# Kernel tuning notes

Measured on AMD Instinct MI355X. Metric: run time of the kernel, lower is better.

Reference implementation:

```python
import jax, jax.numpy as jnp
import numpy as np

B, N, C_IN = 4, 48, 32
HID = [32, 32]          # hidden_channel_list
NB = [32, 32]           # neighborhood_channels
C_OUT = 16
N_BASIS = 6             # equivariant 2->2 basis ops used by SnConv2


def _masked(t, mask):
    # zero out entries for padded nodes; mask: B,n,n,n bool, t: B,n,n,n,C
    return jnp.where(mask[..., None], t, jnp.zeros((), t.dtype))


def snconv2(t, W, b):
    """Sn-equivariant 2nd-order conv on dims (1,2); dim 3 rides along.
    t: B,i,j,m,C.  W: [6, C_in, C_out], one mixing matrix per basis op."""
    n = t.shape[1]
    tT = jnp.swapaxes(t, 1, 2)                       # transpose op
    diag = jnp.einsum('biimc->bimc', t)              # diagonal, B,i,m,C
    rows = t.sum(axis=2) / n                         # row sums,  B,i,m,C
    cols = t.sum(axis=1) / n                         # col sums,  B,j,m,C
    tot = t.sum(axis=(1, 2)) / (n * n)               # total sum, B,m,C
    # contract small features BEFORE broadcasting back to 2nd order
    out = (jnp.einsum('bijmc,cd->bijmd', t, W[0])
           + jnp.einsum('bijmc,cd->bijmd', tT, W[1])
           + jnp.einsum('bimc,cd->bimd', diag, W[2])[:, :, None]
           + jnp.einsum('bimc,cd->bimd', rows, W[3])[:, :, None]
           + jnp.einsum('bjmc,cd->bjmd', cols, W[4])[:, None]
           + jnp.einsum('bmc,cd->bmd', tot, W[5])[:, None, None]
           + b)
    return out


def localconv2(t, Wv, bv, Ww, bw, Wo, bo):
    """LocalConv2, product_type='elementwise': per-channel message passing
    along the node dims: z[b,i,j] = sum_k v[b,i,k] * w[b,k,j] / n."""
    n = t.shape[1]
    v = jnp.einsum('bijmc,cd->bijmd', t, Wv) + bv
    w = jnp.einsum('bijmc,cd->bijmd', t, Ww) + bw
    z = jnp.einsum('bikmc,bkjmc->bijmc', v, w) / n
    return jnp.einsum('bijmc,cd->bijmd', z, Wo) + bo


def setup_inputs() -> dict:
    key = jax.random.key(0)
    ks = jax.random.split(key, 24)
    x = jax.random.normal(ks[0], (B, N, C_IN), dtype=jnp.float32)
    # graphs of unequal size: per-graph node counts in [N//2, N]
    sizes = jax.random.randint(ks[1], (B,), N // 2, N + 1)
    node_valid = jnp.arange(N)[None, :] < sizes[:, None]            # B,n
    mask = (node_valid[:, :, None, None]
            & node_valid[:, None, :, None]
            & node_valid[:, None, None, :])                          # B,n,n,n
    s = 0.05
    inp = {'x': x, 'mask': mask}
    cin = C_IN
    for li, (nch, cout) in enumerate(zip(NB, HID)):
        inp[f'basic_W{li}'] = s * jax.random.normal(ks[2 + 8 * li], (N_BASIS, cin, cin), dtype=jnp.float32)
        inp[f'basic_b{li}'] = jnp.zeros((cin,), jnp.float32)
        inp[f'lv_W{li}'] = s * jax.random.normal(ks[3 + 8 * li], (cin, nch), dtype=jnp.float32)
        inp[f'lv_b{li}'] = jnp.zeros((nch,), jnp.float32)
        inp[f'lw_W{li}'] = s * jax.random.normal(ks[4 + 8 * li], (cin, nch), dtype=jnp.float32)
        inp[f'lw_b{li}'] = jnp.zeros((nch,), jnp.float32)
        inp[f'lo_W{li}'] = s * jax.random.normal(ks[5 + 8 * li], (nch, cout), dtype=jnp.float32)
        inp[f'lo_b{li}'] = jnp.zeros((cout,), jnp.float32)
        cin = cout
    inp['final_W'] = s * jax.random.normal(ks[20], (N_BASIS, cin, C_OUT), dtype=jnp.float32)
    inp['final_b'] = jnp.zeros((C_OUT,), jnp.float32)
    return inp


def reference(x, mask,
              basic_W0, basic_b0, lv_W0, lv_b0, lw_W0, lw_b0, lo_W0, lo_b0,
              basic_W1, basic_b1, lv_W1, lv_b1, lw_W1, lw_b1, lo_W1, lo_b1,
              final_W, final_b):
    # order-3 outer product T[b,i,j,k,c] = x[b,i,c]*x[b,j,c]*x[b,k,c]
    t = (x[:, :, None, None, :] * x[:, None, :, None, :]) * x[:, None, None, :, :]
    t = _masked(t, mask)
    layers = [(basic_W0, basic_b0, lv_W0, lv_b0, lw_W0, lw_b0, lo_W0, lo_b0),
              (basic_W1, basic_b1, lv_W1, lv_b1, lw_W1, lw_b1, lo_W1, lo_b1)]
    for bw_, bb_, vw, vb, ww, wb, ow, ob in layers:
        t = _masked(snconv2(t, bw_, bb_), mask)
        t = localconv2(t, vw, vb, ww, wb, ow, ob)
        t = jax.nn.relu(t)
        t = _masked(t, mask)
    out = _masked(snconv2(t, final_W, final_b), mask)
    return out
```

## Files before the change

### kernel.cpp

```cpp
#include <hip/hip_runtime.h>
#include <cstdint>


namespace {

constexpr int nB = 4, nN = 48, nC = 32;
constexpr int SJ_ = nN * nC;
constexpr int SI_ = nN * SJ_;
constexpr long SB_ = (long)nN * SI_;
constexpr int RP_ = 294912;
constexpr int CP_ = 294912;
constexpr int TP_ = 6144;

__device__ __forceinline__ void decodePos(int p, int& b, int& i, int& j, int& m) {
    m = p % nN; int r = p / nN;
    j = r % nN; r /= nN;
    i = r % nN; b = r / nN;
}

__global__ __launch_bounds__(256) void k_prep(const float* __restrict__ x,
                                              const void* __restrict__ maskp,
                                              float* __restrict__ vm,
                                              float* __restrict__ S)
{
    __shared__ float vmL[nB * nN];
    const int tid = threadIdx.x;
    const unsigned int w0 = *(const unsigned int*)maskp;
    const bool is_byte = (w0 == 0x01010101u);
    if (tid < nB * nN) {
        int b = tid / nN, i = tid % nN;
        long idx = ((long)(b * nN + i) * nN + i) * nN + i;
        int bit;
        if (is_byte) bit = (((const unsigned char*)maskp)[idx] != 0);
        else         bit = (((const int*)maskp)[idx] != 0);
        float f = bit ? 1.f : 0.f;
        vm[tid] = f; vmL[tid] = f;
    }
    __syncthreads();
    if (tid < nB * nC) {
        int b = tid >> 5, c = tid & 31;
        float s = 0.f;
        for (int j = 0; j < nN; ++j) s += x[(b * nN + j) * nC + c] * vmL[b * nN + j];
        S[tid] = s;
    }
}

__global__ __launch_bounds__(256) void k_compose(
    const float* __restrict__ Wb0, const float* __restrict__ bb0,
    const float* __restrict__ Wv0, const float* __restrict__ Ww0,
    const float* __restrict__ Wb1, const float* __restrict__ bb1,
    const float* __restrict__ Wv1, const float* __restrict__ Ww1,
    float* __restrict__ cW, float* __restrict__ cb, float* __restrict__ cWs)
{
    const int blk = blockIdx.x;
    const float* Wb = (blk < 2) ? Wb0 : Wb1;
    const float* bb = (blk < 2) ? bb0 : bb1;
    const float* Wr = (blk == 0) ? Wv0 : (blk == 1) ? Ww0 : (blk == 2) ? Wv1 : Ww1;
    __shared__ float Ws[1024];
    const int tid = threadIdx.x;
    for (int q = tid; q < 1024; q += 256) Ws[q] = Wr[q];
    __syncthreads();
    for (int q = tid; q < 6144; q += 256) {
        const int d = q & 31;
        const float* row = Wb + (q >> 5) * 32;
        float s = 0.f;
        #pragma unroll
        for (int e = 0; e < 32; ++e) s = fmaf(row[e], Ws[e * 32 + d], s);
        cW[blk * 6144 + q] = s;
    }
    if (blk < 2) {
        for (int q = tid; q < 1024; q += 256) {
            const int d = q & 31; const int c = q >> 5;
            const float* r0 = Wb + c * 32;
            const float* r1 = Wb + 1024 + c * 32;
            float s = 0.f;
            #pragma unroll
            for (int e = 0; e < 32; ++e) s = fmaf(r0[e] + r1[e], Ws[e * 32 + d], s);
            cWs[blk * 1024 + q] = s;
        }
    }
    if (tid < 32) {
        float s = 0.f;
        #pragma unroll
        for (int e = 0; e < 32; ++e) s = fmaf(bb[e], Ws[e * 32 + tid], s);
        cb[blk * 32 + tid] = s;
    }
}

__global__ __launch_bounds__(256) void k_mix0(
    const float* __restrict__ x, const float* __restrict__ S,
    const float* __restrict__ Wb, const float* __restrict__ bias,
    float* __restrict__ drp, float* __restrict__ ccp, float* __restrict__ tbp)
{
    __shared__ float W2s[1024], W3s[1024], W4s[1024], W5s[1024], bs[32];
    const int tid = threadIdx.x;
    for (int q = tid; q < 1024; q += 256) {
        W2s[q] = Wb[2048 + q]; W3s[q] = Wb[3072 + q];
        W4s[q] = Wb[4096 + q]; W5s[q] = Wb[5120 + q];
    }
    if (tid < 32) bs[tid] = bias[tid];
    __syncthreads();
    const int id = blockIdx.x * 256 + tid;
    const int m = id % nN; int r = id / nN; const int i = r % nN; const int b = r / nN;
    float odr[32], occ[32];
    #pragma unroll
    for (int d = 0; d < 32; ++d) { odr[d] = 0.f; occ[d] = 0.f; }
    for (int c2 = 0; c2 < 32; ++c2) {
        float xi = x[(b * nN + i) * nC + c2];
        float xm = x[(b * nN + m) * nC + c2];
        float sc = S[b * nC + c2];
        float A = xi * xi * xm;
        float R = xi * xm * sc * (1.f / nN);
        #pragma unroll
        for (int d = 0; d < 32; ++d) {
            odr[d] = fmaf(A, W2s[c2 * 32 + d], fmaf(R, W3s[c2 * 32 + d], odr[d]));
            occ[d] = fmaf(R, W4s[c2 * 32 + d], occ[d]);
        }
    }
    #pragma unroll
    for (int d = 0; d < 32; d += 4) {
        *(float4*)(drp + (size_t)id * 32 + d) = make_float4(odr[d], odr[d+1], odr[d+2], odr[d+3]);
        *(float4*)(ccp + (size_t)id * 32 + d) = make_float4(occ[d], occ[d+1], occ[d+2], occ[d+3]);
    }
    if (i == 0) {
        float ot[32];
        #pragma unroll
        for (int d = 0; d < 32; ++d) ot[d] = bs[d];
        for (int c2 = 0; c2 < 32; ++c2) {
            float xm = x[(b * nN + m) * nC + c2];
            float sc = S[b * nC + c2];
            float Tc = xm * sc * sc * (1.f / (nN * nN));
            #pragma unroll
            for (int d = 0; d < 32; ++d) ot[d] = fmaf(Tc, W5s[c2 * 32 + d], ot[d]);
        }
        for (int d = 0; d < 32; d += 4)
            *(float4*)(tbp + (size_t)(b * nN + m) * 32 + d) = make_float4(ot[d], ot[d+1], ot[d+2], ot[d+3]);
    }
}

template <int DOUT>
__global__ __launch_bounds__(256) void k_mix(
    const float* __restrict__ dgp, const float* __restrict__ rw2,
    const float* __restrict__ cl2, const float* __restrict__ tt4,
    const float* __restrict__ Wb, const float* __restrict__ bias,
    float* __restrict__ drp, float* __restrict__ ccp, float* __restrict__ tbp)
{
    __shared__ float W2s[32 * DOUT], W3s[32 * DOUT], W4s[32 * DOUT], W5s[32 * DOUT], bs[DOUT];
    const int tid = threadIdx.x;
    for (int q = tid; q < 32 * DOUT; q += 256) {
        W2s[q] = Wb[2 * 32 * DOUT + q]; W3s[q] = Wb[3 * 32 * DOUT + q];
        W4s[q] = Wb[4 * 32 * DOUT + q]; W5s[q] = Wb[5 * 32 * DOUT + q];
    }
    if (tid < DOUT) bs[tid] = bias[tid];
    __syncthreads();
    const int id = blockIdx.x * 256 + tid;
    const int m = id % nN; int r = id / nN; const int i = r % nN; const int b = r / nN;
    float odr[DOUT], occ[DOUT];
    #pragma unroll
    for (int d = 0; d < DOUT; ++d) { odr[d] = 0.f; occ[d] = 0.f; }
    for (int c2 = 0; c2 < 32; ++c2) {
        size_t q = (size_t)id * 32 + c2;
        float dg = dgp[q];
        float rw = (rw2[q] + rw2[q + RP_]) * (1.f / nN);
        float cl = (cl2[q] + cl2[q + CP_]) * (1.f / nN);
        #pragma unroll
        for (int d = 0; d < DOUT; ++d) {
            odr[d] = fmaf(dg, W2s[c2 * DOUT + d], fmaf(rw, W3s[c2 * DOUT + d], odr[d]));
            occ[d] = fmaf(cl, W4s[c2 * DOUT + d], occ[d]);
        }
    }
    #pragma unroll
    for (int d = 0; d < DOUT; d += 4) {
        *(float4*)(drp + (size_t)id * DOUT + d) = make_float4(odr[d], odr[d+1], odr[d+2], odr[d+3]);
        *(float4*)(ccp + (size_t)id * DOUT + d) = make_float4(occ[d], occ[d+1], occ[d+2], occ[d+3]);
    }
    if (i == 0) {
        float ot[DOUT];
        #pragma unroll
        for (int d = 0; d < DOUT; ++d) ot[d] = bs[d];
        for (int c2 = 0; c2 < 32; ++c2) {
            size_t q = (size_t)(b * nN + m) * 32 + c2;
            float tv = (tt4[q] + tt4[q + TP_] + tt4[q + 2 * TP_] + tt4[q + 3 * TP_])
                       * (1.f / (nN * nN));
            #pragma unroll
            for (int d = 0; d < DOUT; ++d) ot[d] = fmaf(tv, W5s[c2 * DOUT + d], ot[d]);
        }
        for (int d = 0; d < DOUT; d += 4)
            *(float4*)(tbp + (size_t)(b * nN + m) * DOUT + d) = make_float4(ot[d], ot[d+1], ot[d+2], ot[d+3]);
    }
}

#define FMA4(ar, tv, w4)                       \
    ar[0] = fmaf(tv, w4.x, ar[0]);             \
    ar[1] = fmaf(tv, w4.y, ar[1]);             \
    ar[2] = fmaf(tv, w4.z, ar[2]);             \
    ar[3] = fmaf(tv, w4.w, ar[3]);

template <int MODE>
__global__ __launch_bounds__(256) void k_vw(
    const float* __restrict__ src, const float* __restrict__ vm,
    const float* __restrict__ drv, const float* __restrict__ ccv, const float* __restrict__ tbv,
    const float* __restrict__ drw, const float* __restrict__ ccw, const float* __restrict__ tbw,
    const float* __restrict__ Wv2, const float* __restrict__ Ww2,
    const float* __restrict__ bv, const float* __restrict__ bw,
    float* __restrict__ vout, float* __restrict__ wout)
{
    __shared__ float sA[128 * 34];
    __shared__ float sB[(MODE == 0) ? 4 : 128 * 34];
    __shared__ float wL[(MODE == 0) ? 2048 : 4096];
    const int tid = threadIdx.x;
    const long base = (long)blockIdx.x * 128;

    {
        float4* wl4 = (float4*)wL;
        if (MODE == 0) {
            for (int q = tid; q < 512; q += 256) wl4[q] = ((const float4*)Wv2)[q];
        } else {
            for (int q = tid; q < 512; q += 256) wl4[q] = ((const float4*)Wv2)[q];
            for (int q = tid; q < 512; q += 256) wl4[512 + q] = ((const float4*)Ww2)[q];
        }
    }
    if (MODE == 0) {
        for (int rep = 0; rep < 4; ++rep) {
            int q = rep * 256 + tid; int pl = q >> 3, cq = q & 7;
            int p = (int)base + pl;
            int b, i, j, m; decodePos(p, b, i, j, m);
            float4 xi = *(const float4*)(src + (size_t)(b * nN + i) * nC + cq * 4);
            float4 xj = *(const float4*)(src + (size_t)(b * nN + j) * nC + cq * 4);
            float4 xm = *(const float4*)(src + (size_t)(b * nN + m) * nC + cq * 4);
            int o = pl * 34 + cq * 4;
            sA[o + 0] = xi.x * xj.x * xm.x;
            sA[o + 1] = xi.y * xj.y * xm.y;
            sA[o + 2] = xi.z * xj.z * xm.z;
            sA[o + 3] = xi.w * xj.w * xm.w;
        }
    } else {
        for (int rep = 0; rep < 4; ++rep) {
            int q = rep * 256 + tid; int pl = q >> 3, cq = q & 7;
            long p = base + pl;
            float4 a = *(const float4*)(src + p * nC + cq * 4);
            int o = pl * 34 + cq * 4;
            sA[o + 0] = a.x; sA[o + 1] = a.y; sA[o + 2] = a.z; sA[o + 3] = a.w;
            int b, i, j, m; decodePos((int)p, b, i, j, m);
            long pT = ((long)(b * nN + j) * nN + i) * nN + m;
            float4 t4 = *(const float4*)(src + pT * nC + cq * 4);
            sB[o + 0] = t4.x; sB[o + 1] = t4.y; sB[o + 2] = t4.z; sB[o + 3] = t4.w;
        }
    }
    __syncthreads();

    const int pt = tid >> 3, dq = tid & 7;
    const int p0 = pt * 4, d0 = dq * 4;
    float accv[4][4], accw[4][4];
    #pragma unroll
    for (int l = 0; l < 4; ++l)
        #pragma unroll
        for (int d = 0; d < 4; ++d) { accv[l][d] = 0.f; accw[l][d] = 0.f; }

    auto sweep_dual = [&](const float* sp, const float* wv_, const float* ww_) {
        #pragma unroll
        for (int cp = 0; cp < 16; ++cp) {
            float2 t0 = *(const float2*)(sp + (p0 + 0) * 34 + cp * 2);
            float2 t1 = *(const float2*)(sp + (p0 + 1) * 34 + cp * 2);
            float2 t2 = *(const float2*)(sp + (p0 + 2) * 34 + cp * 2);
            float2 t3 = *(const float2*)(sp + (p0 + 3) * 34 + cp * 2);
            const int c0 = cp * 2, c1 = cp * 2 + 1;
            float4 wv0 = *(const float4*)(wv_ + c0 * nC + d0);
            float4 wv1 = *(const float4*)(wv_ + c1 * nC + d0);
            float4 ww0 = *(const float4*)(ww_ + c0 * nC + d0);
            float4 ww1 = *(const float4*)(ww_ + c1 * nC + d0);
            FMA4(accv[0], t0.x, wv0); FMA4(accv[1], t1.x, wv0);
            FMA4(accv[2], t2.x, wv0); FMA4(accv[3], t3.x, wv0);
            FMA4(accv[0], t0.y, wv1); FMA4(accv[1], t1.y, wv1);
            FMA4(accv[2], t2.y, wv1); FMA4(accv[3], t3.y, wv1);
            FMA4(accw[0], t0.x, ww0); FMA4(accw[1], t1.x, ww0);
            FMA4(accw[2], t2.x, ww0); FMA4(accw[3], t3.x, ww0);
            FMA4(accw[0], t0.y, ww1); FMA4(accw[1], t1.y, ww1);
            FMA4(accw[2], t2.y, ww1); FMA4(accw[3], t3.y, ww1);
        }
    };

    if (MODE == 0) {
        sweep_dual(sA, wL, wL + 1024);
    } else {
        sweep_dual(sA, wL, wL + 2048);
        sweep_dual(sB, wL + 1024, wL + 3072);
    }

    __builtin_amdgcn_sched_barrier(0);
    {
        float4 b4 = *(const float4*)(bv + d0);
        #pragma unroll
        for (int l = 0; l < 4; ++l) {
            int p = (int)base + p0 + l;
            int b, i, j, m; decodePos(p, b, i, j, m);
            float4 d4 = *(const float4*)(drv + (size_t)((b * nN + i) * nN + m) * nC + d0);
            float4 c4 = *(const float4*)(ccv + (size_t)((b * nN + j) * nN + m) * nC + d0);
            float4 t4 = *(const float4*)(tbv + (size_t)(b * nN + m) * nC + d0);
            float mk = vm[b * nN + i] * vm[b * nN + j] * vm[b * nN + m];
            float4 o4;
            o4.x = (accv[l][0] + d4.x + c4.x + t4.x) * mk + b4.x;
            o4.y = (accv[l][1] + d4.y + c4.y + t4.y) * mk + b4.y;
            o4.z = (accv[l][2] + d4.z + c4.z + t4.z) * mk + b4.z;
            o4.w = (accv[l][3] + d4.w + c4.w + t4.w) * mk + b4.w;
            *(float4*)(vout + (size_t)(base + p0 + l) * nC + d0) = o4;
        }
    }
    __builtin_amdgcn_sched_barrier(0);
    {
        float4 b4 = *(const float4*)(bw + d0);
        #pragma unroll
        for (int l = 0; l < 4; ++l) {
            int p = (int)base + p0 + l;
            int b, i, j, m; decodePos(p, b, i, j, m);
            float4 d4 = *(const float4*)(drw + (size_t)((b * nN + i) * nN + m) * nC + d0);
            float4 c4 = *(const float4*)(ccw + (size_t)((b * nN + j) * nN + m) * nC + d0);
            float4 t4 = *(const float4*)(tbw + (size_t)(b * nN + m) * nC + d0);
            float mk = vm[b * nN + i] * vm[b * nN + j] * vm[b * nN + m];
            float4 o4;
            o4.x = (accw[l][0] + d4.x + c4.x + t4.x) * mk + b4.x;
            o4.y = (accw[l][1] + d4.y + c4.y + t4.y) * mk + b4.y;
            o4.z = (accw[l][2] + d4.z + c4.z + t4.z) * mk + b4.z;
            o4.w = (accw[l][3] + d4.w + c4.w + t4.w) * mk + b4.w;
            *(float4*)(wout + (size_t)(base + p0 + l) * nC + d0) = o4;
        }
    }
}

__global__ __launch_bounds__(256, 3) void k_z(
    const float* __restrict__ v, const float* __restrict__ w,
    const float* __restrict__ Wo, const float* __restrict__ bo,
    const float* __restrict__ vm, float* __restrict__ tout,
    float* __restrict__ rows2, float* __restrict__ cols2,
    float* __restrict__ diag_, float* __restrict__ tot4)
{
    __shared__ float lds[12912];
    float* Vt = lds;
    float* Wt = lds + 6456;
    constexpr int ZS = 34;
    constexpr int ZWO = 9792;
    constexpr int TOT0 = 10816;
    const int tid = threadIdx.x;
    const int blk = blockIdx.x;
    const int tl = blk & 3; const int bm = blk >> 2;
    const int it = tl >> 1, jt = tl & 1;
    const int b = bm / nN, m = bm % nN;
    const int c = tid & 31;
    const int g = tid >> 5;
    const int i3 = g >> 1, j2 = g & 1;
    const int il0 = i3 * 6, jl0 = j2 * 12;
    const size_t posbase = (size_t)b * SB_ + (size_t)m * nC;

    float acc[6][12];
    #pragma unroll
    for (int l = 0; l < 6; ++l)
        #pragma unroll
        for (int u = 0; u < 12; ++u) acc[l][u] = 0.f;

    for (int kc = 0; kc < 6; ++kc) {
        if (kc) __syncthreads();
        #pragma unroll
        for (int rr = 0; rr < 6; ++rr) {
            int q = rr * 256 + tid; int pos = q >> 3, cq = q & 7;
            int ii = pos >> 3, kk = pos & 7;
            float4 a = *(const float4*)(v + posbase + (size_t)(it * 24 + ii) * SI_
                                          + (size_t)(kc * 8 + kk) * SJ_ + cq * 4);
            float* dst = Vt + kk * 807 + (cq * 4) * 25 + ii;
            dst[0] = a.x; dst[25] = a.y; dst[50] = a.z; dst[75] = a.w;
        }
        #pragma unroll
        for (int rr = 0; rr < 6; ++rr) {
            int q = rr * 256 + tid; int pos = q >> 3, cq = q & 7;
            int kk = pos / 24, jj = pos - kk * 24;
            float4 a = *(const float4*)(w + posbase + (size_t)(kc * 8 + kk) * SI_
                                          + (size_t)(jt * 24 + jj) * SJ_ + cq * 4);
            float* dst = Wt + kk * 807 + (cq * 4) * 25 + jj;
            dst[0] = a.x; dst[25] = a.y; dst[50] = a.z; dst[75] = a.w;
        }
        __syncthreads();
        #pragma unroll
        for (int kk = 0; kk < 8; ++kk) {
            float vf[6], wf[12];
            #pragma unroll
            for (int l = 0; l < 6; ++l) vf[l] = Vt[kk * 807 + c * 25 + il0 + l];
            #pragma unroll
            for (int u = 0; u < 12; ++u) wf[u] = Wt[kk * 807 + c * 25 + jl0 + u];
            #pragma unroll
            for (int l = 0; l < 6; ++l)
                #pragma unroll
                for (int u = 0; u < 12; ++u)
                    acc[l][u] = fmaf(vf[l], wf[u], acc[l][u]);
        }
    }
    __syncthreads();

    #pragma unroll
    for (int e = 0; e < 4; ++e)
        lds[ZWO + e * 256 + tid] = Wo[e * 256 + tid] * (1.f / nN);

    const int ptE = tid >> 3, dqE = tid & 7, d0 = dqE * 4;
    const float4 b4 = *(const float4*)(bo + d0);
    const float vmm = vm[b * nN + m];
    float colacc[3] = {0.f, 0.f, 0.f};
    float totacc = 0.f;

    for (int h = 0; h < 2; ++h) {
        if (h) __syncthreads();
        if ((i3 >> 1) == h) {
            int r0 = il0 - 12 * h;
            #pragma unroll
            for (int l = 0; l < 6; ++l)
                #pragma unroll
                for (int u = 0; u < 12; ++u)
                    lds[((r0 + l) * 24 + jl0 + u) * ZS + c] = acc[l][u];
        }
        __syncthreads();

        float oac[9][4];
        #pragma unroll
        for (int u = 0; u < 9; ++u)
            #pragma unroll
            for (int d = 0; d < 4; ++d) oac[u][d] = 0.f;
        #pragma unroll
        for (int c2 = 0; c2 < 32; ++c2) {
            float4 wo4 = *(const float4*)(lds + ZWO + c2 * 32 + d0);
            float zv[9];
            #pragma unroll
            for (int u = 0; u < 9; ++u) zv[u] = lds[(ptE * 9 + u) * ZS + c2];
            #pragma unroll
            for (int u = 0; u < 9; ++u) {
                oac[u][0] = fmaf(zv[u], wo4.x, oac[u][0]);
                oac[u][1] = fmaf(zv[u], wo4.y, oac[u][1]);
                oac[u][2] = fmaf(zv[u], wo4.z, oac[u][2]);
                oac[u][3] = fmaf(zv[u], wo4.w, oac[u][3]);
            }
        }
        __syncthreads();

        #pragma unroll
        for (int u = 0; u < 9; ++u) {
            int p = ptE * 9 + u;
            int rl = p / 24, jl = p - rl * 24;
            int gi = it * 24 + 12 * h + rl, gj = jt * 24 + jl;
            float mk = vm[b * nN + gi] * vm[b * nN + gj] * vmm;
            float4 o4;
            o4.x = fmaxf(oac[u][0] + b4.x, 0.f) * mk;
            o4.y = fmaxf(oac[u][1] + b4.y, 0.f) * mk;
            o4.z = fmaxf(oac[u][2] + b4.z, 0.f) * mk;
            o4.w = fmaxf(oac[u][3] + b4.w, 0.f) * mk;
            *(float4*)(tout + posbase + (size_t)gi * SI_ + (size_t)gj * SJ_ + d0) = o4;
            *(float2*)(lds + p * ZS + d0) = make_float2(o4.x, o4.y);
            *(float2*)(lds + p * ZS + d0 + 2) = make_float2(o4.z, o4.w);
        }
        __syncthreads();

        for (int rd = 0; rd < 2; ++rd) {
            int task = rd * 256 + tid;
            if (task < 384) {
                int i_r = task >> 5, c_r = task & 31;
                float rsum = 0.f;
                #pragma unroll
                for (int jl = 0; jl < 24; ++jl) rsum += lds[(i_r * 24 + jl) * ZS + c_r];
                int gi = it * 24 + 12 * h + i_r;
                rows2[(size_t)jt * RP_ + ((size_t)(b * nN + gi) * nN + m) * nC + c_r] = rsum;
                totacc += rsum;
                if (it == jt)
                    diag_[((size_t)(b * nN + gi) * nN + m) * nC + c_r] =
                        lds[(i_r * 24 + (12 * h + i_r)) * ZS + c_r];
            }
        }
        #pragma unroll
        for (int rr = 0; rr < 3; ++rr) {
            int task = rr * 256 + tid;
            int jl = task >> 5, c_c = task & 31;
            float csum = 0.f;
            #pragma unroll
            for (int il = 0; il < 12; ++il) csum += lds[(il * 24 + jl) * ZS + c_c];
            colacc[rr] += csum;
        }
    }

    #pragma unroll
    for (int rr = 0; rr < 3; ++rr) {
        int task = rr * 256 + tid;
        int jl = task >> 5, c_c = task & 31;
        cols2[(size_t)it * CP_ + ((size_t)(b * nN + jt * 24 + jl) * nN + m) * nC + c_c] = colacc[rr];
    }
    lds[TOT0 + g * 32 + c] = totacc;
    __syncthreads();
    if (tid < 32) {
        float s = 0.f;
        #pragma unroll
        for (int gg = 0; gg < 8; ++gg) s += lds[TOT0 + gg * 32 + tid];
        tot4[(size_t)(it * 2 + jt) * TP_ + (size_t)(b * nN + m) * nC + tid] = s;
    }
}

__global__ __launch_bounds__(256) void k_final(
    const float* __restrict__ t, const float* __restrict__ vm,
    const float* __restrict__ drp, const float* __restrict__ ccp, const float* __restrict__ tbp,
    const float* __restrict__ W0, const float* __restrict__ W1,
    float* __restrict__ out)
{
    __shared__ float sA[128 * 34], sB[128 * 34];
    const int tid = threadIdx.x;
    const long base = (long)blockIdx.x * 128;
    for (int rep = 0; rep < 4; ++rep) {
        int q = rep * 256 + tid; int pl = q >> 3, cq = q & 7;
        long p = base + pl;
        float4 a = *(const float4*)(t + p * nC + cq * 4);
        int o = pl * 34 + cq * 4;
        sA[o + 0] = a.x; sA[o + 1] = a.y; sA[o + 2] = a.z; sA[o + 3] = a.w;
        int b, i, j, m; decodePos((int)p, b, i, j, m);
        long pT = ((long)(b * nN + j) * nN + i) * nN + m;
        float4 t4 = *(const float4*)(t + pT * nC + cq * 4);
        sB[o + 0] = t4.x; sB[o + 1] = t4.y; sB[o + 2] = t4.z; sB[o + 3] = t4.w;
    }
    __syncthreads();
    const int pt = tid >> 3, dq = tid & 7;
    const int p0 = pt * 4, d0 = dq * 2;
    float wc[32][2], acc[4][2];
    #pragma unroll
    for (int l = 0; l < 4; ++l) { acc[l][0] = 0.f; acc[l][1] = 0.f; }

    auto loadW = [&](const float* Wp) {
        #pragma unroll
        for (int c2 = 0; c2 < 32; ++c2) {
            float2 q2 = *(const float2*)(Wp + c2 * 16 + d0);
            wc[c2][0] = q2.x; wc[c2][1] = q2.y;
        }
    };
    auto sweep = [&](const float* sp) {
        #pragma unroll
        for (int cp = 0; cp < 16; ++cp) {
            float2 t0 = *(const float2*)(sp + (p0 + 0) * 34 + cp * 2);
            float2 t1 = *(const float2*)(sp + (p0 + 1) * 34 + cp * 2);
            float2 t2 = *(const float2*)(sp + (p0 + 2) * 34 + cp * 2);
            float2 t3 = *(const float2*)(sp + (p0 + 3) * 34 + cp * 2);
            const int c0 = cp * 2, c1 = cp * 2 + 1;
            acc[0][0] = fmaf(t0.x, wc[c0][0], acc[0][0]); acc[0][1] = fmaf(t0.x, wc[c0][1], acc[0][1]);
            acc[1][0] = fmaf(t1.x, wc[c0][0], acc[1][0]); acc[1][1] = fmaf(t1.x, wc[c0][1], acc[1][1]);
            acc[2][0] = fmaf(t2.x, wc[c0][0], acc[2][0]); acc[2][1] = fmaf(t2.x, wc[c0][1], acc[2][1]);
            acc[3][0] = fmaf(t3.x, wc[c0][0], acc[3][0]); acc[3][1] = fmaf(t3.x, wc[c0][1], acc[3][1]);
            acc[0][0] = fmaf(t0.y, wc[c1][0], acc[0][0]); acc[0][1] = fmaf(t0.y, wc[c1][1], acc[0][1]);
            acc[1][0] = fmaf(t1.y, wc[c1][0], acc[1][0]); acc[1][1] = fmaf(t1.y, wc[c1][1], acc[1][1]);
            acc[2][0] = fmaf(t2.y, wc[c1][0], acc[2][0]); acc[2][1] = fmaf(t2.y, wc[c1][1], acc[2][1]);
            acc[3][0] = fmaf(t3.y, wc[c1][0], acc[3][0]); acc[3][1] = fmaf(t3.y, wc[c1][1], acc[3][1]);
        }
    };

    loadW(W0); sweep(sA);
    loadW(W1); sweep(sB);

    #pragma unroll
    for (int l = 0; l < 4; ++l) {
        int p = (int)base + p0 + l;
        int b, i, j, m; decodePos(p, b, i, j, m);
        float2 d2 = *(const float2*)(drp + (size_t)((b * nN + i) * nN + m) * 16 + d0);
        float2 cc2 = *(const float2*)(ccp + (size_t)((b * nN + j) * nN + m) * 16 + d0);
        float2 tb2 = *(const float2*)(tbp + (size_t)(b * nN + m) * 16 + d0);
        float mk = vm[b * nN + i] * vm[b * nN + j] * vm[b * nN + m];
        float2 o2;
        o2.x = (acc[l][0] + d2.x + cc2.x + tb2.x) * mk;
        o2.y = (acc[l][1] + d2.y + cc2.y + tb2.y) * mk;
        *(float2*)(out + (size_t)p * 16 + d0) = o2;
    }
}

}

extern "C" void kernel_launch(void* const* d_in, const int* in_sizes, int n_in,
                              void* d_out, int out_size, void* d_ws, size_t ws_size,
                              hipStream_t stream)
{
    (void)in_sizes; (void)n_in; (void)out_size; (void)ws_size;
    const float* x    = (const float*)d_in[0];
    const void*  mask = d_in[1];
    const float* bW0  = (const float*)d_in[2];
    const float* bb0  = (const float*)d_in[3];
    const float* lvW0 = (const float*)d_in[4];
    const float* lvb0 = (const float*)d_in[5];
    const float* lwW0 = (const float*)d_in[6];
    const float* lwb0 = (const float*)d_in[7];
    const float* loW0 = (const float*)d_in[8];
    const float* lob0 = (const float*)d_in[9];
    const float* bW1  = (const float*)d_in[10];
    const float* bb1  = (const float*)d_in[11];
    const float* lvW1 = (const float*)d_in[12];
    const float* lvb1 = (const float*)d_in[13];
    const float* lwW1 = (const float*)d_in[14];
    const float* lwb1 = (const float*)d_in[15];
    const float* loW1 = (const float*)d_in[16];
    const float* lob1 = (const float*)d_in[17];
    const float* fW   = (const float*)d_in[18];
    const float* fb   = (const float*)d_in[19];

    float* ws  = (float*)d_ws;
    float* t     = ws;
    float* v     = ws + 14155776L;
    float* w     = ws + 28311552L;
    float* rows2 = ws + 42467328L;
    float* cols2 = rows2 + 2 * 294912;
    float* diag  = cols2 + 2 * 294912;
    float* tot4  = diag + 294912;
    float* drv   = tot4 + 4 * 6144;
    float* ccv   = drv + 294912;
    float* tbv   = ccv + 294912;
    float* drw   = tbv + 6144;
    float* ccw   = drw + 294912;
    float* tbw   = ccw + 294912;
    float* cW    = tbw + 6144;
    float* cb    = cW + 4 * 6144;
    float* cWs   = cb + 128;
    float* S     = cWs + 2048;
    float* vm    = S + 128;
    float* out   = (float*)d_out;

    k_prep<<<1, 256, 0, stream>>>(x, mask, vm, S);
    k_compose<<<4, 256, 0, stream>>>(bW0, bb0, lvW0, lwW0, bW1, bb1, lvW1, lwW1, cW, cb, cWs);

    k_mix0<<<36, 256, 0, stream>>>(x, S, cW + 0,    cb + 0,  drv, ccv, tbv);
    k_mix0<<<36, 256, 0, stream>>>(x, S, cW + 6144, cb + 32, drw, ccw, tbw);
    k_vw<0><<<3456, 256, 0, stream>>>(x, vm, drv, ccv, tbv, drw, ccw, tbw,
                                      cWs,
                                      cWs,
                                      lvb0, lwb0, v, w);
    k_z<<<768, 256, 0, stream>>>(v, w, loW0, lob0, vm, t, rows2, cols2, diag, tot4);

    k_mix<32><<<36, 256, 0, stream>>>(diag, rows2, cols2, tot4, cW + 12288, cb + 64, drv, ccv, tbv);
    k_mix<32><<<36, 256, 0, stream>>>(diag, rows2, cols2, tot4, cW + 18432, cb + 96, drw, ccw, tbw);
    k_vw<1><<<3456, 256, 0, stream>>>(t, vm, drv, ccv, tbv, drw, ccw, tbw,
                                      cW + 12288,
                                      cW + 18432,
                                      lvb1, lwb1, v, w);
    k_z<<<768, 256, 0, stream>>>(v, w, loW1, lob1, vm, t, rows2, cols2, diag, tot4);

    k_mix<16><<<36, 256, 0, stream>>>(diag, rows2, cols2, tot4, fW, fb, drv, ccv, tbv);
    k_final<<<3456, 256, 0, stream>>>(t, vm, drv, ccv, tbv, fW, fW + 512, out);
}
```

Baseline: 547.8 us.

## Persistent double-buffered chunk loop in vw/final kernels and merge small launches

The k_vw and k_final kernels become persistent-style blocks. Each block processes 9 chunks of 64 positions with a register-staged double buffer in LDS, so the global loads for the next chunk overlap the FMA sweep on the current one. Grid size drops from 3456 to 768 blocks. Separately, prep and compose are merged into one launch, and the paired mix kernels are merged into single launches with a block-index switch, cutting launch count. The cost is fewer positions per thread per chunk (2 instead of 4), which lowers weight reuse from registers, plus extra register pressure from the staged loads.

```diff
diff --git a/kernel.cpp b/kernel.cpp
--- a/kernel.cpp
+++ b/kernel.cpp
@@ -18,46 +18,45 @@
     i = r % nN; b = r / nN;
 }
 
-__global__ __launch_bounds__(256) void k_prep(const float* __restrict__ x,
-                                              const void* __restrict__ maskp,
-                                              float* __restrict__ vm,
-                                              float* __restrict__ S)
-{
-    __shared__ float vmL[nB * nN];
-    const int tid = threadIdx.x;
-    const unsigned int w0 = *(const unsigned int*)maskp;
-    const bool is_byte = (w0 == 0x01010101u);
-    if (tid < nB * nN) {
-        int b = tid / nN, i = tid % nN;
-        long idx = ((long)(b * nN + i) * nN + i) * nN + i;
-        int bit;
-        if (is_byte) bit = (((const unsigned char*)maskp)[idx] != 0);
-        else         bit = (((const int*)maskp)[idx] != 0);
-        float f = bit ? 1.f : 0.f;
-        vm[tid] = f; vmL[tid] = f;
-    }
-    __syncthreads();
-    if (tid < nB * nC) {
-        int b = tid >> 5, c = tid & 31;
-        float s = 0.f;
-        for (int j = 0; j < nN; ++j) s += x[(b * nN + j) * nC + c] * vmL[b * nN + j];
-        S[tid] = s;
-    }
-}
-
-__global__ __launch_bounds__(256) void k_compose(
+__global__ __launch_bounds__(256) void k_prepcomp(
+    const float* __restrict__ x, const void* __restrict__ maskp,
+    float* __restrict__ vm, float* __restrict__ S,
     const float* __restrict__ Wb0, const float* __restrict__ bb0,
     const float* __restrict__ Wv0, const float* __restrict__ Ww0,
     const float* __restrict__ Wb1, const float* __restrict__ bb1,
     const float* __restrict__ Wv1, const float* __restrict__ Ww1,
     float* __restrict__ cW, float* __restrict__ cb, float* __restrict__ cWs)
 {
+    __shared__ float Ws[1024];
+    __shared__ float vmL[nB * nN];
+    const int tid = threadIdx.x;
+
+    if (blockIdx.x == 4) {
+        const unsigned int w0 = *(const unsigned int*)maskp;
+        const bool is_byte = (w0 == 0x01010101u);
+        if (tid < nB * nN) {
+            int b = tid / nN, i = tid % nN;
+            long idx = ((long)(b * nN + i) * nN + i) * nN + i;
+            int bit;
+            if (is_byte) bit = (((const unsigned char*)maskp)[idx] != 0);
+            else         bit = (((const int*)maskp)[idx] != 0);
+            float f = bit ? 1.f : 0.f;
+            vm[tid] = f; vmL[tid] = f;
+        }
+        __syncthreads();
+        if (tid < nB * nC) {
+            int b = tid >> 5, c = tid & 31;
+            float s = 0.f;
+            for (int j = 0; j < nN; ++j) s += x[(b * nN + j) * nC + c] * vmL[b * nN + j];
+            S[tid] = s;
+        }
+        return;
+    }
+
     const int blk = blockIdx.x;
     const float* Wb = (blk < 2) ? Wb0 : Wb1;
     const float* bb = (blk < 2) ? bb0 : bb1;
     const float* Wr = (blk == 0) ? Wv0 : (blk == 1) ? Ww0 : (blk == 2) ? Wv1 : Ww1;
-    __shared__ float Ws[1024];
-    const int tid = threadIdx.x;
     for (int q = tid; q < 1024; q += 256) Ws[q] = Wr[q];
     __syncthreads();
     for (int q = tid; q < 6144; q += 256) {
@@ -89,9 +88,17 @@
 
 __global__ __launch_bounds__(256) void k_mix0(
     const float* __restrict__ x, const float* __restrict__ S,
-    const float* __restrict__ Wb, const float* __restrict__ bias,
-    float* __restrict__ drp, float* __restrict__ ccp, float* __restrict__ tbp)
+    const float* __restrict__ Wb_a, const float* __restrict__ bias_a,
+    float* __restrict__ dr_a, float* __restrict__ cc_a, float* __restrict__ tb_a,
+    const float* __restrict__ Wb_b, const float* __restrict__ bias_b,
+    float* __restrict__ dr_b, float* __restrict__ cc_b, float* __restrict__ tb_b)
 {
+    const int set = (blockIdx.x >= 36);
+    const float* Wb   = set ? Wb_b   : Wb_a;
+    const float* bias = set ? bias_b : bias_a;
+    float* drp = set ? dr_b : dr_a;
+    float* ccp = set ? cc_b : cc_a;
+    float* tbp = set ? tb_b : tb_a;
     __shared__ float W2s[1024], W3s[1024], W4s[1024], W5s[1024], bs[32];
     const int tid = threadIdx.x;
     for (int q = tid; q < 1024; q += 256) {
@@ -100,7 +107,7 @@
     }
     if (tid < 32) bs[tid] = bias[tid];
     __syncthreads();
-    const int id = blockIdx.x * 256 + tid;
+    const int id = (blockIdx.x - (set ? 36 : 0)) * 256 + tid;
     const int m = id % nN; int r = id / nN; const int i = r % nN; const int b = r / nN;
     float odr[32], occ[32];
     #pragma unroll
@@ -142,9 +149,17 @@
 __global__ __launch_bounds__(256) void k_mix(
     const float* __restrict__ dgp, const float* __restrict__ rw2,
     const float* __restrict__ cl2, const float* __restrict__ tt4,
-    const float* __restrict__ Wb, const float* __restrict__ bias,
-    float* __restrict__ drp, float* __restrict__ ccp, float* __restrict__ tbp)
+    const float* __restrict__ Wb_a, const float* __restrict__ bias_a,
+    float* __restrict__ dr_a, float* __restrict__ cc_a, float* __restrict__ tb_a,
+    const float* __restrict__ Wb_b, const float* __restrict__ bias_b,
+    float* __restrict__ dr_b, float* __restrict__ cc_b, float* __restrict__ tb_b)
 {
+    const int set = (blockIdx.x >= 36);
+    const float* Wb   = set ? Wb_b   : Wb_a;
+    const float* bias = set ? bias_b : bias_a;
+    float* drp = set ? dr_b : dr_a;
+    float* ccp = set ? cc_b : cc_a;
+    float* tbp = set ? tb_b : tb_a;
     __shared__ float W2s[32 * DOUT], W3s[32 * DOUT], W4s[32 * DOUT], W5s[32 * DOUT], bs[DOUT];
     const int tid = threadIdx.x;
     for (int q = tid; q < 32 * DOUT; q += 256) {
@@ -153,7 +168,7 @@
     }
     if (tid < DOUT) bs[tid] = bias[tid];
     __syncthreads();
-    const int id = blockIdx.x * 256 + tid;
+    const int id = (blockIdx.x - (set ? 36 : 0)) * 256 + tid;
     const int m = id % nN; int r = id / nN; const int i = r % nN; const int b = r / nN;
     float odr[DOUT], occ[DOUT];
     #pragma unroll
@@ -205,124 +220,169 @@
     const float* __restrict__ bv, const float* __restrict__ bw,
     float* __restrict__ vout, float* __restrict__ wout)
 {
-    __shared__ float sA[128 * 34];
-    __shared__ float sB[(MODE == 0) ? 4 : 128 * 34];
+    constexpr int CH = 64;
+    constexpr int CS = CH * 34;
+    constexpr int BUF = (MODE == 0) ? CS : 2 * CS;
+    __shared__ float sT[2][BUF];
     __shared__ float wL[(MODE == 0) ? 2048 : 4096];
     const int tid = threadIdx.x;
-    const long base = (long)blockIdx.x * 128;
 
     {
         float4* wl4 = (float4*)wL;
-        if (MODE == 0) {
-            for (int q = tid; q < 512; q += 256) wl4[q] = ((const float4*)Wv2)[q];
-        } else {
-            for (int q = tid; q < 512; q += 256) wl4[q] = ((const float4*)Wv2)[q];
+        for (int q = tid; q < 512; q += 256) wl4[q] = ((const float4*)Wv2)[q];
+        if (MODE == 1)
             for (int q = tid; q < 512; q += 256) wl4[512 + q] = ((const float4*)Ww2)[q];
-        }
-    }
-    if (MODE == 0) {
-        for (int rep = 0; rep < 4; ++rep) {
-            int q = rep * 256 + tid; int pl = q >> 3, cq = q & 7;
-            int p = (int)base + pl;
-            int b, i, j, m; decodePos(p, b, i, j, m);
-            float4 xi = *(const float4*)(src + (size_t)(b * nN + i) * nC + cq * 4);
-            float4 xj = *(const float4*)(src + (size_t)(b * nN + j) * nC + cq * 4);
-            float4 xm = *(const float4*)(src + (size_t)(b * nN + m) * nC + cq * 4);
-            int o = pl * 34 + cq * 4;
-            sA[o + 0] = xi.x * xj.x * xm.x;
-            sA[o + 1] = xi.y * xj.y * xm.y;
-            sA[o + 2] = xi.z * xj.z * xm.z;
-            sA[o + 3] = xi.w * xj.w * xm.w;
-        }
-    } else {
-        for (int rep = 0; rep < 4; ++rep) {
-            int q = rep * 256 + tid; int pl = q >> 3, cq = q & 7;
-            long p = base + pl;
-            float4 a = *(const float4*)(src + p * nC + cq * 4);
-            int o = pl * 34 + cq * 4;
-            sA[o + 0] = a.x; sA[o + 1] = a.y; sA[o + 2] = a.z; sA[o + 3] = a.w;
-            int b, i, j, m; decodePos((int)p, b, i, j, m);
-            long pT = ((long)(b * nN + j) * nN + i) * nN + m;
-            float4 t4 = *(const float4*)(src + pT * nC + cq * 4);
-            sB[o + 0] = t4.x; sB[o + 1] = t4.y; sB[o + 2] = t4.z; sB[o + 3] = t4.w;
-        }
-    }
+    }
+
+    const int base0 = blockIdx.x * 9 * CH;
+    float4 rA0, rA1, rB0, rB1;
+
+    auto loadChunk = [&](int k) {
+        const int cb = base0 + k * CH;
+        {   const int q = tid; const int pl = q >> 3, cq = q & 7;
+            const int p = cb + pl;
+            if (MODE == 0) {
+                int b, i, j, m; decodePos(p, b, i, j, m);
+                float4 xi = *(const float4*)(src + (size_t)(b * nN + i) * nC + cq * 4);
+                float4 xj = *(const float4*)(src + (size_t)(b * nN + j) * nC + cq * 4);
+                float4 xm = *(const float4*)(src + (size_t)(b * nN + m) * nC + cq * 4);
+                rA0.x = xi.x * xj.x * xm.x; rA0.y = xi.y * xj.y * xm.y;
+                rA0.z = xi.z * xj.z * xm.z; rA0.w = xi.w * xj.w * xm.w;
+            } else {
+                rA0 = *(const float4*)(src + (size_t)p * nC + cq * 4);
+                int b, i, j, m; decodePos(p, b, i, j, m);
+                long pT = ((long)(b * nN + j) * nN + i) * nN + m;
+                rB0 = *(const float4*)(src + pT * nC + cq * 4);
+            }
+        }
+        {   const int q = 256 + tid; const int pl = q >> 3, cq = q & 7;
+            const int p = cb + pl;
+            if (MODE == 0) {
+                int b, i, j, m; decodePos(p, b, i, j, m);
+                float4 xi = *(const float4*)(src + (size_t)(b * nN + i) * nC + cq * 4);
+                float4 xj = *(const float4*)(src + (size_t)(b * nN + j) * nC + cq * 4);
+                float4 xm = *(const float4*)(src + (size_t)(b * nN + m) * nC + cq * 4);
+                rA1.x = xi.x * xj.x * xm.x; rA1.y = xi.y * xj.y * xm.y;
+                rA1.z = xi.z * xj.z * xm.z; rA1.w = xi.w * xj.w * xm.w;
+            } else {
+                rA1 = *(const float4*)(src + (size_t)p * nC + cq * 4);
+                int b, i, j, m; decodePos(p, b, i, j, m);
+                long pT = ((long)(b * nN + j) * nN + i) * nN + m;
+                rB1 = *(const float4*)(src + pT * nC + cq * 4);
+            }
+        }
+    };
+    auto writeChunk = [&](int buf) {
+        {   const int q = tid; const int o = (q >> 3) * 34 + (q & 7) * 4;
+            sT[buf][o + 0] = rA0.x; sT[buf][o + 1] = rA0.y;
+            sT[buf][o + 2] = rA0.z; sT[buf][o + 3] = rA0.w;
+            if (MODE == 1) {
+                sT[buf][CS + o + 0] = rB0.x; sT[buf][CS + o + 1] = rB0.y;
+                sT[buf][CS + o + 2] = rB0.z; sT[buf][CS + o + 3] = rB0.w;
+            }
+        }
+        {   const int q = 256 + tid; const int o = (q >> 3) * 34 + (q & 7) * 4;
+            sT[buf][o + 0] = rA1.x; sT[buf][o + 1] = rA1.y;
+            sT[buf][o + 2] = rA1.z; sT[buf][o + 3] = rA1.w;
+            if (MODE == 1) {
+                sT[buf][CS + o + 0] = rB1.x; sT[buf][CS + o + 1] = rB1.y;
+                sT[buf][CS + o + 2] = rB1.z; sT[buf][CS + o + 3] = rB1.w;
+            }
+        }
+    };
+
+    loadChunk(0);
+    writeChunk(0);
     __syncthreads();
 
     const int pt = tid >> 3, dq = tid & 7;
-    const int p0 = pt * 4, d0 = dq * 4;
-    float accv[4][4], accw[4][4];
-    #pragma unroll
-    for (int l = 0; l < 4; ++l)
-        #pragma unroll
-        for (int d = 0; d < 4; ++d) { accv[l][d] = 0.f; accw[l][d] = 0.f; }
-
-    auto sweep_dual = [&](const float* sp, const float* wv_, const float* ww_) {
+    const int p0 = pt * 2, d0 = dq * 4;
+
+    for (int k = 0; k < 9; ++k) {
+        const int cur = k & 1;
+        if (k < 8) loadChunk(k + 1);
+        __builtin_amdgcn_sched_barrier(0);
+
+        float accv[2][4], accw[2][4];
+        #pragma unroll
+        for (int l = 0; l < 2; ++l)
+            #pragma unroll
+            for (int d = 0; d < 4; ++d) { accv[l][d] = 0.f; accw[l][d] = 0.f; }
+
+        const float* sp = sT[cur];
         #pragma unroll
         for (int cp = 0; cp < 16; ++cp) {
             float2 t0 = *(const float2*)(sp + (p0 + 0) * 34 + cp * 2);
             float2 t1 = *(const float2*)(sp + (p0 + 1) * 34 + cp * 2);
-            float2 t2 = *(const float2*)(sp + (p0 + 2) * 34 + cp * 2);
-            float2 t3 = *(const float2*)(sp + (p0 + 3) * 34 + cp * 2);
             const int c0 = cp * 2, c1 = cp * 2 + 1;
-            float4 wv0 = *(const float4*)(wv_ + c0 * nC + d0);
-            float4 wv1 = *(const float4*)(wv_ + c1 * nC + d0);
-            float4 ww0 = *(const float4*)(ww_ + c0 * nC + d0);
-            float4 ww1 = *(const float4*)(ww_ + c1 * nC + d0);
+            const float* wwb = (MODE == 0) ? (wL + 1024) : (wL + 2048);
+            float4 wv0 = *(const float4*)(wL + c0 * nC + d0);
+            float4 wv1 = *(const float4*)(wL + c1 * nC + d0);
+            float4 ww0 = *(const float4*)(wwb + c0 * nC + d0);
+            float4 ww1 = *(const float4*)(wwb + c1 * nC + d0);
             FMA4(accv[0], t0.x, wv0); FMA4(accv[1], t1.x, wv0);
-            FMA4(accv[2], t2.x, wv0); FMA4(accv[3], t3.x, wv0);
             FMA4(accv[0], t0.y, wv1); FMA4(accv[1], t1.y, wv1);
-            FMA4(accv[2], t2.y, wv1); FMA4(accv[3], t3.y, wv1);
             FMA4(accw[0], t0.x, ww0); FMA4(accw[1], t1.x, ww0);
-            FMA4(accw[2], t2.x, ww0); FMA4(accw[3], t3.x, ww0);
             FMA4(accw[0], t0.y, ww1); FMA4(accw[1], t1.y, ww1);
-            FMA4(accw[2], t2.y, ww1); FMA4(accw[3], t3.y, ww1);
-        }
-    };
-
-    if (MODE == 0) {
-        sweep_dual(sA, wL, wL + 1024);
-    } else {
-        sweep_dual(sA, wL, wL + 2048);
-        sweep_dual(sB, wL + 1024, wL + 3072);
-    }
-
-    __builtin_amdgcn_sched_barrier(0);
-    {
-        float4 b4 = *(const float4*)(bv + d0);
-        #pragma unroll
-        for (int l = 0; l < 4; ++l) {
-            int p = (int)base + p0 + l;
-            int b, i, j, m; decodePos(p, b, i, j, m);
-            float4 d4 = *(const float4*)(drv + (size_t)((b * nN + i) * nN + m) * nC + d0);
-            float4 c4 = *(const float4*)(ccv + (size_t)((b * nN + j) * nN + m) * nC + d0);
-            float4 t4 = *(const float4*)(tbv + (size_t)(b * nN + m) * nC + d0);
-            float mk = vm[b * nN + i] * vm[b * nN + j] * vm[b * nN + m];
-            float4 o4;
-            o4.x = (accv[l][0] + d4.x + c4.x + t4.x) * mk + b4.x;
-            o4.y = (accv[l][1] + d4.y + c4.y + t4.y) * mk + b4.y;
-            o4.z = (accv[l][2] + d4.z + c4.z + t4.z) * mk + b4.z;
-            o4.w = (accv[l][3] + d4.w + c4.w + t4.w) * mk + b4.w;
-            *(float4*)(vout + (size_t)(base + p0 + l) * nC + d0) = o4;
-        }
-    }
-    __builtin_amdgcn_sched_barrier(0);
-    {
-        float4 b4 = *(const float4*)(bw + d0);
-        #pragma unroll
-        for (int l = 0; l < 4; ++l) {
-            int p = (int)base + p0 + l;
-            int b, i, j, m; decodePos(p, b, i, j, m);
-            float4 d4 = *(const float4*)(drw + (size_t)((b * nN + i) * nN + m) * nC + d0);
-            float4 c4 = *(const float4*)(ccw + (size_t)((b * nN + j) * nN + m) * nC + d0);
-            float4 t4 = *(const float4*)(tbw + (size_t)(b * nN + m) * nC + d0);
-            float mk = vm[b * nN + i] * vm[b * nN + j] * vm[b * nN + m];
-            float4 o4;
-            o4.x = (accw[l][0] + d4.x + c4.x + t4.x) * mk + b4.x;
-            o4.y = (accw[l][1] + d4.y + c4.y + t4.y) * mk + b4.y;
-            o4.z = (accw[l][2] + d4.z + c4.z + t4.z) * mk + b4.z;
-            o4.w = (accw[l][3] + d4.w + c4.w + t4.w) * mk + b4.w;
-            *(float4*)(wout + (size_t)(base + p0 + l) * nC + d0) = o4;
+        }
+        if (MODE == 1) {
+            #pragma unroll
+            for (int cp = 0; cp < 16; ++cp) {
+                float2 t0 = *(const float2*)(sp + CS + (p0 + 0) * 34 + cp * 2);
+                float2 t1 = *(const float2*)(sp + CS + (p0 + 1) * 34 + cp * 2);
+                const int c0 = cp * 2, c1 = cp * 2 + 1;
+                float4 wv0 = *(const float4*)(wL + 1024 + c0 * nC + d0);
+                float4 wv1 = *(const float4*)(wL + 1024 + c1 * nC + d0);
+                float4 ww0 = *(const float4*)(wL + 3072 + c0 * nC + d0);
+                float4 ww1 = *(const float4*)(wL + 3072 + c1 * nC + d0);
+                FMA4(accv[0], t0.x, wv0); FMA4(accv[1], t1.x, wv0);
+                FMA4(accv[0], t0.y, wv1); FMA4(accv[1], t1.y, wv1);
+                FMA4(accw[0], t0.x, ww0); FMA4(accw[1], t1.x, ww0);
+                FMA4(accw[0], t0.y, ww1); FMA4(accw[1], t1.y, ww1);
+            }
+        }
+
+        const int cb = base0 + k * CH;
+        {
+            float4 b4 = *(const float4*)(bv + d0);
+            #pragma unroll
+            for (int l = 0; l < 2; ++l) {
+                int p = cb + p0 + l;
+                int b, i, j, m; decodePos(p, b, i, j, m);
+                float4 d4 = *(const float4*)(drv + (size_t)((b * nN + i) * nN + m) * nC + d0);
+                float4 c4 = *(const float4*)(ccv + (size_t)((b * nN + j) * nN + m) * nC + d0);
+                float4 t4 = *(const float4*)(tbv + (size_t)(b * nN + m) * nC + d0);
+                float mk = vm[b * nN + i] * vm[b * nN + j] * vm[b * nN + m];
+                float4 o4;
+                o4.x = (accv[l][0] + d4.x + c4.x + t4.x) * mk + b4.x;
+                o4.y = (accv[l][1] + d4.y + c4.y + t4.y) * mk + b4.y;
+                o4.z = (accv[l][2] + d4.z + c4.z + t4.z) * mk + b4.z;
+                o4.w = (accv[l][3] + d4.w + c4.w + t4.w) * mk + b4.w;
+                *(float4*)(vout + (size_t)p * nC + d0) = o4;
+            }
+        }
+        {
+            float4 b4 = *(const float4*)(bw + d0);
+            #pragma unroll
+            for (int l = 0; l < 2; ++l) {
+                int p = cb + p0 + l;
+                int b, i, j, m; decodePos(p, b, i, j, m);
+                float4 d4 = *(const float4*)(drw + (size_t)((b * nN + i) * nN + m) * nC + d0);
+                float4 c4 = *(const float4*)(ccw + (size_t)((b * nN + j) * nN + m) * nC + d0);
+                float4 t4 = *(const float4*)(tbw + (size_t)(b * nN + m) * nC + d0);
+                float mk = vm[b * nN + i] * vm[b * nN + j] * vm[b * nN + m];
+                float4 o4;
+                o4.x = (accw[l][0] + d4.x + c4.x + t4.x) * mk + b4.x;
+                o4.y = (accw[l][1] + d4.y + c4.y + t4.y) * mk + b4.y;
+                o4.z = (accw[l][2] + d4.z + c4.z + t4.z) * mk + b4.z;
+                o4.w = (accw[l][3] + d4.w + c4.w + t4.w) * mk + b4.w;
+                *(float4*)(wout + (size_t)p * nC + d0) = o4;
+            }
+        }
+
+        if (k < 8) {
+            writeChunk((k + 1) & 1);
+            __syncthreads();
         }
     }
 }
@@ -502,68 +562,111 @@
     const float* __restrict__ W0, const float* __restrict__ W1,
     float* __restrict__ out)
 {
-    __shared__ float sA[128 * 34], sB[128 * 34];
+    constexpr int CH = 64, CS = CH * 34;
+    __shared__ float sT[2][2 * CS];
+    __shared__ float wL[1024];
     const int tid = threadIdx.x;
-    const long base = (long)blockIdx.x * 128;
-    for (int rep = 0; rep < 4; ++rep) {
-        int q = rep * 256 + tid; int pl = q >> 3, cq = q & 7;
-        long p = base + pl;
-        float4 a = *(const float4*)(t + p * nC + cq * 4);
-        int o = pl * 34 + cq * 4;
-        sA[o + 0] = a.x; sA[o + 1] = a.y; sA[o + 2] = a.z; sA[o + 3] = a.w;
-        int b, i, j, m; decodePos((int)p, b, i, j, m);
-        long pT = ((long)(b * nN + j) * nN + i) * nN + m;
-        float4 t4 = *(const float4*)(t + pT * nC + cq * 4);
-        sB[o + 0] = t4.x; sB[o + 1] = t4.y; sB[o + 2] = t4.z; sB[o + 3] = t4.w;
-    }
+
+    {
+        float4* wl4 = (float4*)wL;
+        for (int q = tid; q < 128; q += 256) wl4[q] = ((const float4*)W0)[q];
+        for (int q = tid; q < 128; q += 256) wl4[128 + q] = ((const float4*)W1)[q];
+    }
+
+    const int base0 = blockIdx.x * 9 * CH;
+    float4 rA0, rA1, rB0, rB1;
+
+    auto loadChunk = [&](int k) {
+        const int cb = base0 + k * CH;
+        {   const int q = tid; const int pl = q >> 3, cq = q & 7;
+            const int p = cb + pl;
+            rA0 = *(const float4*)(t + (size_t)p * nC + cq * 4);
+            int b, i, j, m; decodePos(p, b, i, j, m);
+            long pT = ((long)(b * nN + j) * nN + i) * nN + m;
+            rB0 = *(const float4*)(t + pT * nC + cq * 4);
+        }
+        {   const int q = 256 + tid; const int pl = q >> 3, cq = q & 7;
+            const int p = cb + pl;
+            rA1 = *(const float4*)(t + (size_t)p * nC + cq * 4);
+            int b, i, j, m; decodePos(p, b, i, j, m);
+            long pT = ((long)(b * nN + j) * nN + i) * nN + m;
+            rB1 = *(const float4*)(t + pT * nC + cq * 4);
+        }
+    };
+    auto writeChunk = [&](int buf) {
+        {   const int q = tid; const int o = (q >> 3) * 34 + (q & 7) * 4;
+            sT[buf][o + 0] = rA0.x; sT[buf][o + 1] = rA0.y;
+            sT[buf][o + 2] = rA0.z; sT[buf][o + 3] = rA0.w;
+            sT[buf][CS + o + 0] = rB0.x; sT[buf][CS + o + 1] = rB0.y;
+            sT[buf][CS + o + 2] = rB0.z; sT[buf][CS + o + 3] = rB0.w;
+        }
+        {   const int q = 256 + tid; const int o = (q >> 3) * 34 + (q & 7) * 4;
+            sT[buf][o + 0] = rA1.x; sT[buf][o + 1] = rA1.y;
+            sT[buf][o + 2] = rA1.z; sT[buf][o + 3] = rA1.w;
+            sT[buf][CS + o + 0] = rB1.x; sT[buf][CS + o + 1] = rB1.y;
+            sT[buf][CS + o + 2] = rB1.z; sT[buf][CS + o + 3] = rB1.w;
+        }
+    };
+
+    loadChunk(0);
+    writeChunk(0);
     __syncthreads();
+
     const int pt = tid >> 3, dq = tid & 7;
-    const int p0 = pt * 4, d0 = dq * 2;
-    float wc[32][2], acc[4][2];
-    #pragma unroll
-    for (int l = 0; l < 4; ++l) { acc[l][0] = 0.f; acc[l][1] = 0.f; }
-
-    auto loadW = [&](const float* Wp) {
-        #pragma unroll
-        for (int c2 = 0; c2 < 32; ++c2) {
-            float2 q2 = *(const float2*)(Wp + c2 * 16 + d0);
-            wc[c2][0] = q2.x; wc[c2][1] = q2.y;
-        }
-    };
-    auto sweep = [&](const float* sp) {
+    const int p0 = pt * 2, d0 = dq * 2;
+
+    for (int k = 0; k < 9; ++k) {
+        const int cur = k & 1;
+        if (k < 8) loadChunk(k + 1);
+        __builtin_amdgcn_sched_barrier(0);
+
+        float acc[2][2];
+        acc[0][0] = 0.f; acc[0][1] = 0.f; acc[1][0] = 0.f; acc[1][1] = 0.f;
+        const float* sp = sT[cur];
         #pragma unroll
         for (int cp = 0; cp < 16; ++cp) {
             float2 t0 = *(const float2*)(sp + (p0 + 0) * 34 + cp * 2);
             float2 t1 = *(const float2*)(sp + (p0 + 1) * 34 + cp * 2);
-            float2 t2 = *(const float2*)(sp + (p0 + 2) * 34 + cp * 2);
-            float2 t3 = *(const float2*)(sp + (p0 + 3) * 34 + cp * 2);
             const int c0 = cp * 2, c1 = cp * 2 + 1;
-            acc[0][0] = fmaf(t0.x, wc[c0][0], acc[0][0]); acc[0][1] = fmaf(t0.x, wc[c0][1], acc[0][1]);
-            acc[1][0] = fmaf(t1.x, wc[c0][0], acc[1][0]); acc[1][1] = fmaf(t1.x, wc[c0][1], acc[1][1]);
-            acc[2][0] = fmaf(t2.x, wc[c0][0], acc[2][0]); acc[2][1] = fmaf(t2.x, wc[c0][1], acc[2][1]);
-            acc[3][0] = fmaf(t3.x, wc[c0][0], acc[3][0]); acc[3][1] = fmaf(t3.x, wc[c0][1], acc[3][1]);
-            acc[0][0] = fmaf(t0.y, wc[c1][0], acc[0][0]); acc[0][1] = fmaf(t0.y, wc[c1][1], acc[0][1]);
-            acc[1][0] = fmaf(t1.y, wc[c1][0], acc[1][0]); acc[1][1] = fmaf(t1.y, wc[c1][1], acc[1][1]);
-            acc[2][0] = fmaf(t2.y, wc[c1][0], acc[2][0]); acc[2][1] = fmaf(t2.y, wc[c1][1], acc[2][1]);
-            acc[3][0] = fmaf(t3.y, wc[c1][0], acc[3][0]); acc[3][1] = fmaf(t3.y, wc[c1][1], acc[3][1]);
-        }
-    };
-
-    loadW(W0); sweep(sA);
-    loadW(W1); sweep(sB);
-
-    #pragma unroll
-    for (int l = 0; l < 4; ++l) {
-        int p = (int)base + p0 + l;
-        int b, i, j, m; decodePos(p, b, i, j, m);
-        float2 d2 = *(const float2*)(drp + (size_t)((b * nN + i) * nN + m) * 16 + d0);
-        float2 cc2 = *(const float2*)(ccp + (size_t)((b * nN + j) * nN + m) * 16 + d0);
-        float2 tb2 = *(const float2*)(tbp + (size_t)(b * nN + m) * 16 + d0);
-        float mk = vm[b * nN + i] * vm[b * nN + j] * vm[b * nN + m];
-        float2 o2;
-        o2.x = (acc[l][0] + d2.x + cc2.x + tb2.x) * mk;
-        o2.y = (acc[l][1] + d2.y + cc2.y + tb2.y) * mk;
-        *(float2*)(out + (size_t)p * 16 + d0) = o2;
+            float2 w0 = *(const float2*)(wL + c0 * 16 + d0);
+            float2 w1 = *(const float2*)(wL + c1 * 16 + d0);
+            acc[0][0] = fmaf(t0.x, w0.x, acc[0][0]); acc[0][1] = fmaf(t0.x, w0.y, acc[0][1]);
+            acc[1][0] = fmaf(t1.x, w0.x, acc[1][0]); acc[1][1] = fmaf(t1.x, w0.y, acc[1][1]);
+            acc[0][0] = fmaf(t0.y, w1.x, acc[0][0]); acc[0][1] = fmaf(t0.y, w1.y, acc[0][1]);
+            acc[1][0] = fmaf(t1.y, w1.x, acc[1][0]); acc[1][1] = fmaf(t1.y, w1.y, acc[1][1]);
+        }
+        #pragma unroll
+        for (int cp = 0; cp < 16; ++cp) {
+            float2 t0 = *(const float2*)(sp + CS + (p0 + 0) * 34 + cp * 2);
+            float2 t1 = *(const float2*)(sp + CS + (p0 + 1) * 34 + cp * 2);
+            const int c0 = cp * 2, c1 = cp * 2 + 1;
+            float2 w0 = *(const float2*)(wL + 512 + c0 * 16 + d0);
+            float2 w1 = *(const float2*)(wL + 512 + c1 * 16 + d0);
+            acc[0][0] = fmaf(t0.x, w0.x, acc[0][0]); acc[0][1] = fmaf(t0.x, w0.y, acc[0][1]);
+            acc[1][0] = fmaf(t1.x, w0.x, acc[1][0]); acc[1][1] = fmaf(t1.x, w0.y, acc[1][1]);
+            acc[0][0] = fmaf(t0.y, w1.x, acc[0][0]); acc[0][1] = fmaf(t0.y, w1.y, acc[0][1]);
+            acc[1][0] = fmaf(t1.y, w1.x, acc[1][0]); acc[1][1] = fmaf(t1.y, w1.y, acc[1][1]);
+        }
+
+        const int cb = base0 + k * CH;
+        #pragma unroll
+        for (int l = 0; l < 2; ++l) {
+            int p = cb + p0 + l;
+            int b, i, j, m; decodePos(p, b, i, j, m);
+            float2 d2 = *(const float2*)(drp + (size_t)((b * nN + i) * nN + m) * 16 + d0);
+            float2 cc2 = *(const float2*)(ccp + (size_t)((b * nN + j) * nN + m) * 16 + d0);
+            float2 tb2 = *(const float2*)(tbp + (size_t)(b * nN + m) * 16 + d0);
+            float mk = vm[b * nN + i] * vm[b * nN + j] * vm[b * nN + m];
+            float2 o2;
+            o2.x = (acc[l][0] + d2.x + cc2.x + tb2.x) * mk;
+            o2.y = (acc[l][1] + d2.y + cc2.y + tb2.y) * mk;
+            *(float2*)(out + (size_t)p * 16 + d0) = o2;
+        }
+
+        if (k < 8) {
+            writeChunk((k + 1) & 1);
+            __syncthreads();
+        }
     }
 }
 
@@ -616,25 +719,30 @@
     float* vm    = S + 128;
     float* out   = (float*)d_out;
 
-    k_prep<<<1, 256, 0, stream>>>(x, mask, vm, S);
-    k_compose<<<4, 256, 0, stream>>>(bW0, bb0, lvW0, lwW0, bW1, bb1, lvW1, lwW1, cW, cb, cWs);
-
-    k_mix0<<<36, 256, 0, stream>>>(x, S, cW + 0,    cb + 0,  drv, ccv, tbv);
-    k_mix0<<<36, 256, 0, stream>>>(x, S, cW + 6144, cb + 32, drw, ccw, tbw);
-    k_vw<0><<<3456, 256, 0, stream>>>(x, vm, drv, ccv, tbv, drw, ccw, tbw,
-                                      cWs,
-                                      cWs,
-                                      lvb0, lwb0, v, w);
+    k_prepcomp<<<5, 256, 0, stream>>>(x, mask, vm, S,
+                                      bW0, bb0, lvW0, lwW0,
+                                      bW1, bb1, lvW1, lwW1, cW, cb, cWs);
+
+    k_mix0<<<72, 256, 0, stream>>>(x, S,
+                                   cW + 0,    cb + 0,  drv, ccv, tbv,
+                                   cW + 6144, cb + 32, drw, ccw, tbw);
+    k_vw<0><<<768, 256, 0, stream>>>(x, vm, drv, ccv, tbv, drw, ccw, tbw,
+                                     cWs,
+                                     cWs,
+                                     lvb0, lwb0, v, w);
     k_z<<<768, 256, 0, stream>>>(v, w, loW0, lob0, vm, t, rows2, cols2, diag, tot4);
 
-    k_mix<32><<<36, 256, 0, stream>>>(diag, rows2, cols2, tot4, cW + 12288, cb + 64, drv, ccv, tbv);
-    k_mix<32><<<36, 256, 0, stream>>>(diag, rows2, cols2, tot4, cW + 18432, cb + 96, drw, ccw, tbw);
-    k_vw<1><<<3456, 256, 0, stream>>>(t, vm, drv, ccv, tbv, drw, ccw, tbw,
-                                      cW + 12288,
-                                      cW + 18432,
-                                      lvb1, lwb1, v, w);
+    k_mix<32><<<72, 256, 0, stream>>>(diag, rows2, cols2, tot4,
+                                      cW + 12288, cb + 64, drv, ccv, tbv,
+                                      cW + 18432, cb + 96, drw, ccw, tbw);
+    k_vw<1><<<768, 256, 0, stream>>>(t, vm, drv, ccv, tbv, drw, ccw, tbw,
+                                     cW + 12288,
+                                     cW + 18432,
+                                     lvb1, lwb1, v, w);
     k_z<<<768, 256, 0, stream>>>(v, w, loW1, lob1, vm, t, rows2, cols2, diag, tot4);
 
-    k_mix<16><<<36, 256, 0, stream>>>(diag, rows2, cols2, tot4, fW, fb, drv, ccv, tbv);
-    k_final<<<3456, 256, 0, stream>>>(t, vm, drv, ccv, tbv, fW, fW + 512, out);
-}
+    k_mix<16><<<36, 256, 0, stream>>>(diag, rows2, cols2, tot4,
+                                      fW, fb, drv, ccv, tbv,
+                                      fW, fb, drv, ccv, tbv);
+    k_final<<<768, 256, 0, stream>>>(t, vm, drv, ccv, tbv, fW, fW + 512, out);
+}
```

Result: faster. 497.7 us (-9.1%).
